# Optimization experiments

Measured on AMD Instinct MI355X. Metric: run time of the kernel, lower is better.

Reference implementation:

```python
import jax, jax.numpy as jnp
import numpy as np

ENC, PRED, H, V, DMAX = 1024, 640, 640, 1024, 4
B, T, U = 4, 256, 64


def setup_inputs() -> dict:
    key = jax.random.key(0)
    ks = jax.random.split(key, 10)
    s = lambda d: 1.0 / np.sqrt(d)
    return {
        "encoder_out": jax.random.normal(ks[0], (B, T, ENC), jnp.float32),
        "predictor_out": jax.random.normal(ks[1], (B, U, PRED), jnp.float32),
        "W_enc": jax.random.uniform(ks[2], (H, ENC), jnp.float32, -s(ENC), s(ENC)),
        "b_enc": jax.random.uniform(ks[3], (H,), jnp.float32, -s(ENC), s(ENC)),
        "W_pred": jax.random.uniform(ks[4], (H, PRED), jnp.float32, -s(PRED), s(PRED)),
        "b_pred": jax.random.uniform(ks[5], (H,), jnp.float32, -s(PRED), s(PRED)),
        "W_out": jax.random.uniform(ks[6], (V, H), jnp.float32, -s(H), s(H)),
        "b_out": jax.random.uniform(ks[7], (V,), jnp.float32, -s(H), s(H)),
        "W_dur": jax.random.uniform(ks[8], (DMAX + 1, H), jnp.float32, -s(H), s(H)),
        "b_dur": jax.random.uniform(ks[9], (DMAX + 1,), jnp.float32, -s(H), s(H)),
    }


def reference(encoder_out, predictor_out, W_enc, b_enc, W_pred, b_pred,
              W_out, b_out, W_dur, b_dur):
    # Project encoder [B,T,H] and predictor [B,U,H]
    enc = jnp.einsum('bte,he->bth', encoder_out, W_enc) + b_enc
    pred = jnp.einsum('bup,hp->buh', predictor_out, W_pred) + b_pred
    # Broadcast-add -> [B,T,U,H], tanh
    joint = jnp.tanh(enc[:, :, None, :] + pred[:, None, :, :])
    # Dual heads
    logits = jnp.einsum('btuh,vh->btuv', joint, W_out) + b_out        # [B,T,U,V]
    durations = jnp.einsum('btuh,dh->btud', joint, W_dur) + b_dur     # [B,T,U,DMAX+1]
    return (logits, durations)
```

## Files before the change

### kernel.cpp

```cpp
#include <hip/hip_runtime.h>

typedef unsigned short u16;
typedef unsigned int u32;

typedef __bf16 bf16x8 __attribute__((ext_vector_type(8)));
typedef float f32x4 __attribute__((ext_vector_type(4)));

union FragI { int4 i; bf16x8 b; u16 u[8]; };

__device__ __forceinline__ u16 f2bf(float x) {
  u32 u = __float_as_uint(x);
  u32 r = (u + 0x7fffu + ((u >> 16) & 1u)) >> 16;
  return (u16)r;
}
__device__ __forceinline__ float tanh_fast(float x) {
  float e = __expf(2.0f * x);
  return 1.0f - __fdividef(2.0f, e + 1.0f);
}
__device__ __forceinline__ bf16x8 load_cvt8(const float* __restrict__ p) {
  float4 f0 = *(const float4*)p;
  float4 f1 = *(const float4*)(p + 4);
  union { bf16x8 b; u16 u[8]; } t;
  t.u[0] = f2bf(f0.x); t.u[1] = f2bf(f0.y); t.u[2] = f2bf(f0.z); t.u[3] = f2bf(f0.w);
  t.u[4] = f2bf(f1.x); t.u[5] = f2bf(f1.y); t.u[6] = f2bf(f1.z); t.u[7] = f2bf(f1.w);
  return t.b;
}

#define GLDS(gptr, lptr) \
  __builtin_amdgcn_global_load_lds((const __attribute__((address_space(1))) u32*)(gptr), \
                                   (__attribute__((address_space(3))) u32*)(lptr), 16, 0, 0)

#define LOGITS_N 67108864

__device__ __forceinline__ void proj_body(const float* __restrict__ A,
                                          const float* __restrict__ Bw,
                                          const float* __restrict__ bias,
                                          float* __restrict__ C,
                                          int m0, int n0, int N, int K,
                                          float (*red)[64][64]) {
  int tid = threadIdx.x;
  int lane = tid & 63, wid = tid >> 6;
  int kper = K >> 2;
  int kbase = wid * kper;
  int ksteps = kper >> 5;
  int r16 = lane & 15, khi = (lane >> 4) * 8;

  f32x4 z = {0.f, 0.f, 0.f, 0.f};
  f32x4 acc[4][4];
  for (int i = 0; i < 4; ++i)
    for (int j = 0; j < 4; ++j) acc[i][j] = z;

  for (int ks = 0; ks < ksteps; ++ks) {
    int k = kbase + ks * 32 + khi;
    bf16x8 af[4], bf[4];
#pragma unroll
    for (int fm = 0; fm < 4; ++fm)
      af[fm] = load_cvt8(A + (size_t)(m0 + fm * 16 + r16) * K + k);
#pragma unroll
    for (int fn = 0; fn < 4; ++fn)
      bf[fn] = load_cvt8(Bw + (size_t)(n0 + fn * 16 + r16) * K + k);
#pragma unroll
    for (int fm = 0; fm < 4; ++fm)
#pragma unroll
      for (int fn = 0; fn < 4; ++fn)
        acc[fm][fn] = __builtin_amdgcn_mfma_f32_16x16x32_bf16(af[fm], bf[fn], acc[fm][fn], 0, 0, 0);
  }

#pragma unroll
  for (int fm = 0; fm < 4; ++fm)
#pragma unroll
    for (int fn = 0; fn < 4; ++fn)
#pragma unroll
      for (int i = 0; i < 4; ++i)
        red[wid][fm * 16 + (lane >> 4) * 4 + i][fn * 16 + r16] = acc[fm][fn][i];
  __syncthreads();
  for (int idx = tid; idx < 4096; idx += 256) {
    int r = idx >> 6, c = idx & 63;
    float s = red[0][r][c] + red[1][r][c] + red[2][r][c] + red[3][r][c] + bias[n0 + c];
    C[(size_t)(m0 + r) * N + n0 + c] = s;
  }
}

__global__ __launch_bounds__(256) void prep(const float* __restrict__ W_out, u16* __restrict__ WoB,
                                            const float* __restrict__ W_dur, u16* __restrict__ WdB,
                                            const float* __restrict__ encoder,
                                            const float* __restrict__ W_enc, const float* __restrict__ b_enc,
                                            float* __restrict__ encP,
                                            const float* __restrict__ predictor,
                                            const float* __restrict__ W_pred, const float* __restrict__ b_pred,
                                            float* __restrict__ predP) {
  __shared__ float red[4][64][64];
  int bx = blockIdx.x;
  int tid = threadIdx.x;
  if (bx < 640) {
    int i = bx * 256 + tid;
    float4 f = ((const float4*)W_out)[i];
    union { u16 u[4]; int2 v; } o;
    o.u[0] = f2bf(f.x); o.u[1] = f2bf(f.y); o.u[2] = f2bf(f.z); o.u[3] = f2bf(f.w);
    ((int2*)WoB)[i] = o.v;
  } else if (bx < 680) {
    int i = (bx - 640) * 256 + tid;
    if (i < 16 * 640) WdB[i] = (i < 5 * 640) ? f2bf(W_dur[i]) : (u16)0;
  } else if (bx < 840) {
    int idx = bx - 680;
    proj_body(encoder, W_enc, b_enc, encP, (idx / 10) * 64, (idx % 10) * 64, 640, 1024, red);
  } else {
    int idx = bx - 840;
    proj_body(predictor, W_pred, b_pred, predP, (idx / 10) * 64, (idx % 10) * 64, 640, 640, red);
  }
}

__global__ __launch_bounds__(256) void joint_tanh(const float* __restrict__ enc,
                                                  const float* __restrict__ pred,
                                                  u16* __restrict__ J) {
  const int total = 65536 * 80;
  for (int c = blockIdx.x * 256 + threadIdx.x; c < total; c += gridDim.x * 256) {
    int m = c / 80;
    int j = c - m * 80;
    int bt = m >> 6;
    int uu = m & 63;
    int b = bt >> 8;
    const float* ep = enc + bt * 640 + j * 8;
    const float* pp = pred + (b * 64 + uu) * 640 + j * 8;
    float4 e0 = *(const float4*)ep;
    float4 e1 = *(const float4*)(ep + 4);
    float4 p0 = *(const float4*)pp;
    float4 p1 = *(const float4*)(pp + 4);
    union { u16 u[8]; int4 v; } o;
    o.u[0] = f2bf(tanh_fast(e0.x + p0.x));
    o.u[1] = f2bf(tanh_fast(e0.y + p0.y));
    o.u[2] = f2bf(tanh_fast(e0.z + p0.z));
    o.u[3] = f2bf(tanh_fast(e0.w + p0.w));
    o.u[4] = f2bf(tanh_fast(e1.x + p1.x));
    o.u[5] = f2bf(tanh_fast(e1.y + p1.y));
    o.u[6] = f2bf(tanh_fast(e1.z + p1.z));
    o.u[7] = f2bf(tanh_fast(e1.w + p1.w));
    *(int4*)(J + (size_t)c * 8) = o.v;
  }
}


__device__ __forceinline__ void stage128(const u16* __restrict__ g, u16* l,
                                         int wid, int lane) {
  int rl = wid * 8 + (lane >> 3);
  int cl = ((lane & 7) ^ (lane >> 3)) * 8;
  const u16* gp = g + (size_t)rl * 640 + cl;
  u16* lp = l + wid * 512;
#pragma unroll
  for (int j = 0; j < 4; ++j)
    GLDS(gp + (size_t)j * 32 * 640, lp + j * 2048);
}

__global__ __launch_bounds__(256, 3) void main_gemm(const u16* __restrict__ J,
                                                    const u16* __restrict__ Wo,
                                                    const u16* __restrict__ Wd,
                                                    const float* __restrict__ b_out,
                                                    const float* __restrict__ b_dur,
                                                    float* __restrict__ out) {
  __shared__ __align__(16) u16 As[8192];
  __shared__ __align__(16) u16 Bs[8192];
  int tid = threadIdx.x;
  int lane = tid & 63, wid = tid >> 6;
  int bid = blockIdx.x;
  int swz = (bid & 7) * 512 + (bid >> 3);
  int bn = swz & 7, bm = swz >> 3;
  int m0 = bm * 128, n0 = bn * 128;
  int wr = wid >> 1, wc = wid & 1;
  int r16 = lane & 15, khi = (lane >> 4) * 8;
  int xorv = (r16 & 7) << 3;
  bool do_dur = (bn == 0);

  f32x4 z = {0.f, 0.f, 0.f, 0.f};
  f32x4 acc[4][4];
#pragma unroll
  for (int i = 0; i < 4; ++i)
#pragma unroll
    for (int j = 0; j < 4; ++j) acc[i][j] = z;
  f32x4 dacc[4] = {z, z, z, z};

  const u16* Jb = J + (size_t)m0 * 640;
  const u16* Wb = Wo + (size_t)n0 * 640;

  for (int t = 0; t < 10; ++t) {
    stage128(Jb + t * 64, As, wid, lane);
    stage128(Wb + t * 64, Bs, wid, lane);
    __syncthreads();
#pragma unroll
    for (int ks = 0; ks < 2; ++ks) {
      int cks = (ks * 32 + khi) ^ xorv;
      FragI af[4], bfr[4], wd;
#pragma unroll
      for (int fn = 0; fn < 4; ++fn)
        bfr[fn].i = *(const int4*)(Bs + (wc * 64 + fn * 16 + r16) * 64 + cks);
#pragma unroll
      for (int fm = 0; fm < 4; ++fm)
        af[fm].i = *(const int4*)(As + (wr * 64 + fm * 16 + r16) * 64 + cks);
      if (do_dur)
        wd.i = *(const int4*)(Wd + (size_t)r16 * 640 + t * 64 + ks * 32 + khi);
#pragma unroll
      for (int fm = 0; fm < 4; ++fm) {
#pragma unroll
        for (int fn = 0; fn < 4; ++fn)
          acc[fm][fn] = __builtin_amdgcn_mfma_f32_16x16x32_bf16(af[fm].b, bfr[fn].b, acc[fm][fn], 0, 0, 0);
        if (do_dur)
          dacc[fm] = __builtin_amdgcn_mfma_f32_16x16x32_bf16(af[fm].b, wd.b, dacc[fm], 0, 0, 0);
      }
    }
    __syncthreads();
  }

  int rb = m0 + wr * 64 + (lane >> 4) * 4;
  int cb = n0 + wc * 64 + r16;
#pragma unroll
  for (int fn = 0; fn < 4; ++fn) {
    int col = cb + fn * 16;
    float bo = b_out[col];
#pragma unroll
    for (int fm = 0; fm < 4; ++fm) {
      int row = rb + fm * 16;
#pragma unroll
      for (int i = 0; i < 4; ++i)
        out[(size_t)(row + i) * 1024 + col] = acc[fm][fn][i] + bo;
    }
  }
  if (do_dur && r16 < 5) {
    float bd = b_dur[r16];
#pragma unroll
    for (int fm = 0; fm < 4; ++fm) {
      int row = rb + fm * 16;
#pragma unroll
      for (int i = 0; i < 4; ++i)
        out[LOGITS_N + (size_t)(row + i) * 5 + r16] = dacc[fm][i] + bd;
    }
  }
}

extern "C" void kernel_launch(void* const* d_in, const int* in_sizes, int n_in,
                              void* d_out, int out_size, void* d_ws, size_t ws_size,
                              hipStream_t stream) {
  const float* encoder   = (const float*)d_in[0];
  const float* predictor = (const float*)d_in[1];
  const float* W_enc = (const float*)d_in[2];
  const float* b_enc = (const float*)d_in[3];
  const float* W_pred = (const float*)d_in[4];
  const float* b_pred = (const float*)d_in[5];
  const float* W_out = (const float*)d_in[6];
  const float* b_out = (const float*)d_in[7];
  const float* W_dur = (const float*)d_in[8];
  const float* b_dur = (const float*)d_in[9];
  float* out = (float*)d_out;

  char* ws = (char*)d_ws;
  u16* Jbuf    = (u16*)(ws);
  u16* WoutB   = (u16*)(ws + 83886080);
  u16* WdurB   = (u16*)(ws + 85196800);
  float* encP  = (float*)(ws + 85217280);
  float* predP = (float*)(ws + 87838720);

  prep<<<880, 256, 0, stream>>>(W_out, WoutB, W_dur, WdurB,
                                encoder, W_enc, b_enc, encP,
                                predictor, W_pred, b_pred, predP);
  joint_tanh<<<2048, 256, 0, stream>>>(encP, predP, Jbuf);
  main_gemm<<<4096, 256, 0, stream>>>(Jbuf, WoutB, WdurB, b_out, b_dur, out);
}
```

Baseline: 172.5 us.

## Double-buffer LDS tiles with K=32 stages and manual vmcnt waits

Replaces the single-buffered K=64 LDS staging with two K=32 buffers. The loads for step t+2 are issued while step t computes, and explicit s_waitcnt vmcnt and s_barrier replace __syncthreads. The LDS swizzle changes to suit 32-element rows. The goal is to hide global-to-LDS latency behind MFMA work. The cost is twice as many barrier iterations and a narrower K slice per step, with the same LDS footprint.

```diff
diff --git a/kernel.cpp b/kernel.cpp
--- a/kernel.cpp
+++ b/kernel.cpp
@@ -140,15 +140,14 @@
 }
 
 
-__device__ __forceinline__ void stage128(const u16* __restrict__ g, u16* l,
-                                         int wid, int lane) {
-  int rl = wid * 8 + (lane >> 3);
-  int cl = ((lane & 7) ^ (lane >> 3)) * 8;
-  const u16* gp = g + (size_t)rl * 640 + cl;
-  u16* lp = l + wid * 512;
-#pragma unroll
-  for (int j = 0; j < 4; ++j)
-    GLDS(gp + (size_t)j * 32 * 640, lp + j * 2048);
+__device__ __forceinline__ void stage32k(const u16* __restrict__ g, u16* l, int tid,
+                                         int wid) {
+#pragma unroll
+  for (int j = 0; j < 2; ++j) {
+    int rl = j * 64 + (tid >> 2);
+    int lc = (tid & 3) ^ ((rl >> 1) & 3);
+    GLDS(g + (size_t)rl * 640 + lc * 8, l + j * 2048 + wid * 512);
+  }
 }
 
 __global__ __launch_bounds__(256, 3) void main_gemm(const u16* __restrict__ J,
@@ -157,8 +156,8 @@
                                                     const float* __restrict__ b_out,
                                                     const float* __restrict__ b_dur,
                                                     float* __restrict__ out) {
-  __shared__ __align__(16) u16 As[8192];
-  __shared__ __align__(16) u16 Bs[8192];
+  __shared__ __align__(16) u16 As[2][4096];
+  __shared__ __align__(16) u16 Bs[2][4096];
   int tid = threadIdx.x;
   int lane = tid & 63, wid = tid >> 6;
   int bid = blockIdx.x;
@@ -166,8 +165,9 @@
   int bn = swz & 7, bm = swz >> 3;
   int m0 = bm * 128, n0 = bn * 128;
   int wr = wid >> 1, wc = wid & 1;
-  int r16 = lane & 15, khi = (lane >> 4) * 8;
-  int xorv = (r16 & 7) << 3;
+  int r16 = lane & 15, g4 = lane >> 4, khi8 = g4 * 8;
+  int xv = (r16 >> 1) & 3;
+  int ckoff = ((g4 ^ xv) * 8);
   bool do_dur = (bn == 0);
 
   f32x4 z = {0.f, 0.f, 0.f, 0.f};
@@ -180,36 +180,55 @@
 
   const u16* Jb = J + (size_t)m0 * 640;
   const u16* Wb = Wo + (size_t)n0 * 640;
-
-  for (int t = 0; t < 10; ++t) {
-    stage128(Jb + t * 64, As, wid, lane);
-    stage128(Wb + t * 64, Bs, wid, lane);
-    __syncthreads();
-#pragma unroll
-    for (int ks = 0; ks < 2; ++ks) {
-      int cks = (ks * 32 + khi) ^ xorv;
-      FragI af[4], bfr[4], wd;
+  const u16* Wdp = Wd + (size_t)r16 * 640 + khi8;
+
+  stage32k(Jb + 0, As[0], tid, wid);
+  stage32k(Wb + 0, Bs[0], tid, wid);
+  stage32k(Jb + 32, As[1], tid, wid);
+  stage32k(Wb + 32, Bs[1], tid, wid);
+
+  for (int t = 0; t < 20; ++t) {
+    const int p = t & 1;
+    if (t < 19) {
+      asm volatile("s_waitcnt vmcnt(4)" ::: "memory");
+    } else {
+      asm volatile("s_waitcnt vmcnt(0)" ::: "memory");
+    }
+    __builtin_amdgcn_sched_barrier(0);
+    __builtin_amdgcn_s_barrier();
+    __builtin_amdgcn_sched_barrier(0);
+
+    FragI af[4], bfr[4], wd;
+#pragma unroll
+    for (int fn = 0; fn < 4; ++fn)
+      bfr[fn].i = *(const int4*)(Bs[p] + (wc * 64 + fn * 16 + r16) * 32 + ckoff);
+#pragma unroll
+    for (int fm = 0; fm < 4; ++fm)
+      af[fm].i = *(const int4*)(As[p] + (wr * 64 + fm * 16 + r16) * 32 + ckoff);
+    if (do_dur)
+      wd.i = *(const int4*)(Wdp + t * 32);
+#pragma unroll
+    for (int fm = 0; fm < 4; ++fm) {
 #pragma unroll
       for (int fn = 0; fn < 4; ++fn)
-        bfr[fn].i = *(const int4*)(Bs + (wc * 64 + fn * 16 + r16) * 64 + cks);
-#pragma unroll
-      for (int fm = 0; fm < 4; ++fm)
-        af[fm].i = *(const int4*)(As + (wr * 64 + fm * 16 + r16) * 64 + cks);
+        acc[fm][fn] = __builtin_amdgcn_mfma_f32_16x16x32_bf16(af[fm].b, bfr[fn].b, acc[fm][fn], 0, 0, 0);
       if (do_dur)
-        wd.i = *(const int4*)(Wd + (size_t)r16 * 640 + t * 64 + ks * 32 + khi);
-#pragma unroll
-      for (int fm = 0; fm < 4; ++fm) {
-#pragma unroll
-        for (int fn = 0; fn < 4; ++fn)
-          acc[fm][fn] = __builtin_amdgcn_mfma_f32_16x16x32_bf16(af[fm].b, bfr[fn].b, acc[fm][fn], 0, 0, 0);
-        if (do_dur)
-          dacc[fm] = __builtin_amdgcn_mfma_f32_16x16x32_bf16(af[fm].b, wd.b, dacc[fm], 0, 0, 0);
+        dacc[fm] = __builtin_amdgcn_mfma_f32_16x16x32_bf16(af[fm].b, wd.b, dacc[fm], 0, 0, 0);
+    }
+
+    if (t < 19) {
+      __builtin_amdgcn_sched_barrier(0);
+      asm volatile("s_waitcnt lgkmcnt(0)" ::: "memory");
+      __builtin_amdgcn_s_barrier();
+      __builtin_amdgcn_sched_barrier(0);
+      if (t + 2 < 20) {
+        stage32k(Jb + (t + 2) * 32, As[p], tid, wid);
+        stage32k(Wb + (t + 2) * 32, Bs[p], tid, wid);
       }
     }
-    __syncthreads();
-  }
-
-  int rb = m0 + wr * 64 + (lane >> 4) * 4;
+  }
+
+  int rb = m0 + wr * 64 + g4 * 4;
   int cb = n0 + wc * 64 + r16;
 #pragma unroll
   for (int fn = 0; fn < 4; ++fn) {
```

New measurement: 185.0 us. 7.2% more time.
